# Kernel optimization log

Hardware: AMD Instinct MI355X
Metric: run time of the kernel (lower is better)

## Reference

```python
import jax, jax.numpy as jnp
import numpy as np

D = 256          # descriptor_dim
H = 4            # num heads in AttentionPropagation
DH = D // H
SCALE = 0.1      # hparams['scale_factor']
THR = 0.2        # hparams['match_threshold']
NAMES = ['GATs', 'self', 'cross'] * 4


def conv1d(x, w, b):
    # 1x1 Conv1d == per-position matmul. x:[b,c,n] w:[o,c] b:[o]
    return jnp.einsum('oc,bcn->bon', w, x) + b[None, :, None]


def instnorm(x, eps=1e-5):
    # torch InstanceNorm1d (affine=False): normalize over spatial dim per channel
    mu = jnp.mean(x, axis=2, keepdims=True)
    var = jnp.var(x, axis=2, keepdims=True)
    return (x - mu) * jax.lax.rsqrt(var + eps)


def linear_attention(q, k, v):
    # q:[b,dh,h,nq] k,v:[b,dh,h,ns]
    eps = 1e-6
    q = jax.nn.elu(q) + 1.0
    k = jax.nn.elu(k) + 1.0
    m = v.shape[3]
    v = v / m
    KV = jnp.einsum('bdhm,bqhm->bqdh', k, v)
    Z = 1.0 / (jnp.einsum('bdhm,bdh->bhm', q, k.sum(3)) + eps)
    return jnp.einsum('bdhm,bqdh,bhm->bqhm', q, KV, Z) * m


def mha(x, src, pw, pb, mw, mb):
    b, _, nq = x.shape
    ns = src.shape[2]
    q = conv1d(x, pw[0], pb[0]).reshape(b, DH, H, nq)
    k = conv1d(src, pw[1], pb[1]).reshape(b, DH, H, ns)
    v = conv1d(src, pw[2], pb[2]).reshape(b, DH, H, ns)
    o = linear_attention(q, k, v).reshape(b, D, nq)
    return conv1d(o, mw, mb)


def attn_prop(x, src, pw, pb, mw, mb, w1, b1, w2, b2):
    msg = mha(x, src, pw, pb, mw, mb)
    y = jnp.concatenate([x, msg], axis=1)           # [b, 2D, n]
    y = jax.nn.relu(instnorm(conv1d(y, w1, b1)))
    return conv1d(y, w2, b2)


def gat(d2d, d3d, W, a):
    # GraphAttentionLayer (OnePose): include_self=True, additional=False,
    # with_linear_transform=True, concat=True; dropout inactive at eval.
    # d2d:[b,D,n*L] d3d:[b,D,n]
    b, _, n = d3d.shape
    x2 = jnp.transpose(d2d, (0, 2, 1)).reshape(b, n, -1, D)   # [b,n,L,D]
    x3 = jnp.transpose(d3d, (0, 2, 1))                        # [b,n,D]
    x2 = jnp.concatenate([x3[:, :, None, :], x2], axis=2)     # include self -> L+1
    Wh2 = jnp.einsum('bnld,do->bnlo', x2, W)
    Wh3 = jnp.einsum('bnd,do->bno', x3, W)
    e = jax.nn.leaky_relu(
        jnp.einsum('bno,o->bn', Wh3, a[:D])[:, :, None]
        + jnp.einsum('bnlo,o->bnl', Wh2, a[D:]), 0.2)
    att = jax.nn.softmax(e, axis=-1)
    h = jnp.einsum('bnl,bnld->bnd', att, Wh2)
    return jnp.transpose(jax.nn.elu(h), (0, 2, 1))            # [b,D,n]


def gnn_and_scores(dq, d3, d2db, projw, projb, mergew, mergeb,
                   mlp1w, mlp1b, mlp2w, mlp2b, gatW, gata, finw, finb):
    gi = 0
    ai = 0
    for name in NAMES:
        if name == 'GATs':
            d3 = gat(d2db, d3, gatW[gi], gata[gi])
            gi += 1
        else:
            src0, src1 = (d3, dq) if name == 'cross' else (dq, d3)
            p = (projw[ai], projb[ai], mergew[ai], mergeb[ai],
                 mlp1w[ai], mlp1b[ai], mlp2w[ai], mlp2b[ai])
            dq = dq + attn_prop(dq, src0, *p)
            d3 = d3 + attn_prop(d3, src1, *p)
            ai += 1
    mq = conv1d(dq, finw, finb)
    md = conv1d(d3, finw, finb)
    mq = mq / jnp.maximum(jnp.linalg.norm(mq, axis=1, keepdims=True), 1e-12)
    md = md / jnp.maximum(jnp.linalg.norm(md, axis=1, keepdims=True), 1e-12)
    scores = jnp.einsum('bdn,bdm->bnm', mq, md) / SCALE
    conf = jax.nn.softmax(scores, axis=1) * jax.nn.softmax(scores, axis=2)
    return conf


def setup_inputs() -> dict:
    key = jax.random.key(0)
    ks = jax.random.split(key, 16)
    b, n1, n2, L = 2, 3072, 3072, 8
    s = 0.02
    f32 = jnp.float32
    return {
        'desc2d_query': jax.random.normal(ks[0], (b, D, n1), f32),
        'desc3d_db': jax.random.normal(ks[1], (b, D, n2), f32),
        'desc2d_db': jax.random.normal(ks[2], (b, D, n2 * L), f32),
        'projw': jax.random.normal(ks[3], (8, 3, D, D), f32) * s,
        'projb': jnp.zeros((8, 3, D), f32),
        'mergew': jax.random.normal(ks[4], (8, D, D), f32) * s,
        'mergeb': jnp.zeros((8, D), f32),
        'mlp1w': jax.random.normal(ks[5], (8, 2 * D, 2 * D), f32) * s,
        'mlp1b': jnp.zeros((8, 2 * D), f32),
        'mlp2w': jax.random.normal(ks[6], (8, D, 2 * D), f32) * s,
        'mlp2b': jnp.zeros((8, D), f32),
        'gatW': jax.random.normal(ks[7], (4, D, D), f32) * s,
        'gata': jax.random.normal(ks[8], (4, 2 * D), f32) * s,
        'finw': jax.random.normal(ks[9], (D, D), f32) * s,
        'finb': jnp.zeros((D,), f32),
    }


def reference(desc2d_query, desc3d_db, desc2d_db, projw, projb, mergew, mergeb,
              mlp1w, mlp1b, mlp2w, mlp2b, gatW, gata, finw, finb):
    conf = gnn_and_scores(desc2d_query, desc3d_db, desc2d_db, projw, projb,
                          mergew, mergeb, mlp1w, mlp1b, mlp2w, mlp2b,
                          gatW, gata, finw, finb)
    b, n1, n2 = conf.shape
    i0 = jnp.argmax(conf, axis=2)
    m0 = jnp.max(conf, axis=2)
    i1 = jnp.argmax(conf, axis=1)
    m1 = jnp.max(conf, axis=1)
    mutual0 = jnp.arange(n1)[None] == jnp.take_along_axis(i1, i0, axis=1)
    mutual1 = jnp.arange(n2)[None] == jnp.take_along_axis(i0, i1, axis=1)
    ms0 = jnp.where(mutual0, m0, 0.0)
    ms1 = jnp.where(mutual1, jnp.take_along_axis(ms0, i1, axis=1), 0.0)
    valid0 = mutual0 & (ms0 > THR)
    valid1 = mutual1 & jnp.take_along_axis(valid0, i1, axis=1)
    ind0 = jnp.where(valid0, i0, -1)
    ind1 = jnp.where(valid1, i1, -1)
    return (ind0[0], ind1[0], ms0[0], ms1[0], conf)
```

## Files before the change

### kernel.cpp

```cpp
#include <hip/hip_runtime.h>
#include <hip/hip_bf16.h>
#include <math.h>

typedef long long ll;
typedef __attribute__((ext_vector_type(8))) short s8v;
typedef __attribute__((ext_vector_type(4))) float f4v;
typedef __attribute__((address_space(1))) unsigned int gu32;
typedef __attribute__((address_space(3))) unsigned int lu32;

#define NPOS 3072

#define OFF_STF   0LL
#define OFF_STB   3145728LL
#define OFF_QKV   4718592LL
#define OFF_MSG   9437184LL
#define OFF_HID   11010048LL
#define OFF_WBF   14155776LL
#define OFF_PBP   16941056LL
#define OFF_KV    16947200LL
#define OFF_KSUM  17012736LL
#define OFF_KSP   17013760LL
#define OFF_UVEC  17026048LL
#define OFF_E2ALL 17028096LL
#define OFF_ATT   17224704LL
#define OFF_SVEC  17280000LL
#define OFF_INP   17292288LL
#define OFF_PMAX  17300480LL
#define OFF_PSUM  17595392LL
#define OFF_CMAX  17890304LL
#define OFF_CSUM  17896448LL
#define OFF_CAPV  17902592LL
#define OFF_CAPI  17976320LL
#define OFF_I0    18050048LL
#define OFF_M0    18053120LL
#define OFF_I1    18056192LL
#define OFF_M1B   18059264LL
#define OFF_B1C   18583552LL

__device__ __forceinline__ float b2f(short s) {
  union { unsigned u; float f; } c;
  c.u = ((unsigned)(unsigned short)s) << 16;
  return c.f;
}
__device__ __forceinline__ short f2b(float f) {
  __hip_bfloat16 h = __float2bfloat16(f);
  union { __hip_bfloat16 h; short s; } c; c.h = h; return c.s;
}
__device__ __forceinline__ unsigned pk2(float a, float b) {
  return (unsigned)(unsigned short)f2b(a) | ((unsigned)(unsigned short)f2b(b) << 16);
}
__device__ __forceinline__ float waveSum(float v) {
#pragma unroll
  for (int off = 32; off > 0; off >>= 1) v += __shfl_down(v, off);
  return v;
}
__device__ __forceinline__ void gld16(const short* g, short* l) {
  __builtin_amdgcn_global_load_lds((const gu32*)g, (lu32*)l, 16, 0, 0);
}

__global__ __launch_bounds__(256) void bgemm_k(
    const short* __restrict__ A, const short* __restrict__ A2, int KS,
    int lda, int lda2,
    const short* __restrict__ B,
    const float* __restrict__ bias, const float* __restrict__ R,
    float* __restrict__ C, short* __restrict__ C2,
    const float* __restrict__ rs, const float* __restrict__ cs,
    int K, int ldc, float alpha,
    ll aB, ll a2B, ll bB, ll rB, ll cB, ll c2B,
    int za, int zbo, int act, int zand)
{
  __shared__ __align__(16) short As[2][128 * 32];
  __shared__ __align__(16) short Bs[2][128 * 32];
  const int z = blockIdx.z;
  const int zA = (z + za) & zand, zB = (z + zbo) & zand;
  const int j0 = blockIdx.x * 128, i0 = blockIdx.y * 128;
  const int t = threadIdx.x;
  const int lane = t & 63, w = t >> 6;
  const int wi = (w & 1) * 64, wj = (w >> 1) * 64;
  const int fr = lane & 15;
  const int cl = lane >> 4;
  const int r4 = cl * 4;

  const short* baseA[2]; const short* baseA2[2]; const short* baseB[2];
  int sl[2];
  {
    const short* Az = A + (ll)zA * aB;
    const short* A2z = A2 ? A2 + (ll)zA * a2B : nullptr;
    const short* Bz = B + (ll)zB * bB;
#pragma unroll
    for (int i = 0; i < 2; ++i) {
      int cc = t + i * 256;
      int r = cc >> 2;
      int sq = ((cc & 3) ^ ((r >> 1) & 3)) << 3;
      baseA[i] = Az + (ll)(i0 + r) * lda + sq;
      baseA2[i] = A2 ? A2z + (ll)(i0 + r) * lda2 + sq : nullptr;
      baseB[i] = Bz + (ll)(j0 + r) * K + sq;
      sl[i] = cc << 3;
    }
  }
  int offA[4], offB[4];
#pragma unroll
  for (int im = 0; im < 4; ++im) {
    int ra = wi + im * 16 + fr;
    offA[im] = ra * 32 + ((cl ^ ((ra >> 1) & 3)) << 3);
    int rb = wj + im * 16 + fr;
    offB[im] = rb * 32 + ((cl ^ ((rb >> 1) & 3)) << 3);
  }

  f4v acc[4][4];
#pragma unroll
  for (int i = 0; i < 4; ++i)
#pragma unroll
    for (int j = 0; j < 4; ++j) acc[i][j] = (f4v)0.f;

  const int nt = K >> 5;
#pragma unroll
  for (int i = 0; i < 2; ++i) gld16(baseA[i], As[0] + sl[i]);
#pragma unroll
  for (int i = 0; i < 2; ++i) gld16(baseB[i], Bs[0] + sl[i]);
  __syncthreads();

  for (int kt = 0; kt < nt; ++kt) {
    const int cur = kt & 1;
    if (kt + 1 < nt) {
      const int k0 = (kt + 1) * 32;
      short* dA = As[cur ^ 1]; short* dB = Bs[cur ^ 1];
      if (A2 && k0 >= KS) {
#pragma unroll
        for (int i = 0; i < 2; ++i) gld16(baseA2[i] + (k0 - KS), dA + sl[i]);
      } else {
#pragma unroll
        for (int i = 0; i < 2; ++i) gld16(baseA[i] + k0, dA + sl[i]);
      }
#pragma unroll
      for (int i = 0; i < 2; ++i) gld16(baseB[i] + k0, dB + sl[i]);
    }
    const short* Ac = As[cur]; const short* Bc = Bs[cur];
    s8v af[4], bfr[4];
#pragma unroll
    for (int im = 0; im < 4; ++im) af[im] = *(const s8v*)(Ac + offA[im]);
#pragma unroll
    for (int in = 0; in < 4; ++in) bfr[in] = *(const s8v*)(Bc + offB[in]);
#pragma unroll
    for (int im = 0; im < 4; ++im)
#pragma unroll
      for (int in = 0; in < 4; ++in)
        acc[im][in] = __builtin_amdgcn_mfma_f32_16x16x32_bf16(
            af[im], bfr[in], acc[im][in], 0, 0, 0);
    __syncthreads();
  }

  float* Cz = C ? C + (ll)z * cB : nullptr;
  short* C2z = C2 ? C2 + (ll)z * c2B : nullptr;
  const float* Rz = R ? R + (ll)z * rB : nullptr;
  const float* rsz = rs ? rs + (ll)z * NPOS : nullptr;
  float bv4[4], cv4[4];
#pragma unroll
  for (int in = 0; in < 4; ++in) {
    int j = j0 + wj + in * 16 + fr;
    bv4[in] = bias ? bias[j] : 0.f;
    cv4[in] = cs ? cs[(ll)zB * NPOS + j] : 1.f;
  }
#pragma unroll
  for (int im = 0; im < 4; ++im) {
#pragma unroll
    for (int r = 0; r < 4; ++r) {
      int i = i0 + wi + im * 16 + r4 + r;
      float rsv = rsz ? rsz[i] : 1.f;
      int rowo = i * ldc;
#pragma unroll
      for (int in = 0; in < 4; ++in) {
        int j = j0 + wj + in * 16 + fr;
        float v = acc[im][in][r] * alpha;
        if (rsz) v = v * rsv * cv4[in];
        v += bv4[in];
        int off = rowo + j;
        if (Rz) v += Rz[off];
        if (act) v = v > 0.f ? v : (expf(v) - 1.f);
        if (Cz) Cz[off] = v;
        if (C2z) C2z[off] = f2b(v);
      }
    }
  }
}

__global__ void transpose_in_k(const float* __restrict__ dq, const float* __restrict__ d3,
                               float* __restrict__ stf, short* __restrict__ stb)
{
  __shared__ float tile[64][65];
  int z = blockIdx.z;
  const float* src = (z < 2) ? dq + (ll)z * 786432 : d3 + (ll)(z - 2) * 786432;
  int c0 = blockIdx.y * 64, n0 = blockIdx.x * 64;
  int t = threadIdx.x;
  int nj = t & 63, q = t >> 6;
#pragma unroll
  for (int i = 0; i < 16; ++i) {
    int ci = q + i * 4;
    tile[ci][nj] = src[(ll)(c0 + ci) * NPOS + n0 + nj];
  }
  __syncthreads();
  int cj = t & 63;
#pragma unroll
  for (int i = 0; i < 16; ++i) {
    int ni = q + i * 4;
    float v = tile[cj][ni];
    ll o = (ll)z * 786432 + (ll)(n0 + ni) * 256 + c0 + cj;
    stf[o] = v;
    stb[o] = f2b(v);
  }
}

__global__ void f2b_k(const float* __restrict__ src, short* __restrict__ dst, int n8)
{
  int gi = blockIdx.x * 256 + threadIdx.x;
  if (gi >= n8) return;
  ll e = (ll)gi * 8;
  float4 a = *(const float4*)(src + e);
  float4 b = *(const float4*)(src + e + 4);
  uint4 o;
  o.x = pk2(a.x, a.y); o.y = pk2(a.z, a.w);
  o.z = pk2(b.x, b.y); o.w = pk2(b.z, b.w);
  *(uint4*)(dst + e) = o;
}

__global__ void f2b_split_k(const float* __restrict__ src, short* __restrict__ d1,
                            short* __restrict__ d2)
{
  int gi = blockIdx.x * 256 + threadIdx.x;
  ll e = (ll)gi * 8;
  int k = (int)(e & 511);
  ll row = e >> 9;
  float4 a = *(const float4*)(src + e);
  float4 b = *(const float4*)(src + e + 4);
  uint4 o;
  o.x = pk2(a.x, a.y); o.y = pk2(a.z, a.w);
  o.z = pk2(b.x, b.y); o.w = pk2(b.z, b.w);
  if (k < 256) *(uint4*)(d1 + row * 512 + k) = o;
  else         *(uint4*)(d2 + row * 256 + (k - 256)) = o;
}

__global__ void projw_perm_k(const float* __restrict__ src, short* __restrict__ dst)
{
  int idx = blockIdx.x * 256 + threadIdx.x;
  int c = idx & 255;
  int row = (idx >> 8) % 768;
  int ai = (idx >> 8) / 768;
  int sec = row >> 8;
  int p = row & 255;
  int o = (p & 63) * 4 + (p >> 6);
  dst[idx] = f2b(src[(((ll)ai * 3 + sec) * 256 + o) * 256 + c]);
}

__global__ void pbp_k(const float* __restrict__ pb, float* __restrict__ pbp)
{
  int idx = blockIdx.x * 256 + threadIdx.x;
  int row = idx % 768, ai = idx / 768;
  int sec = row >> 8;
  int p = row & 255;
  int o = (p & 63) * 4 + (p >> 6);
  pbp[idx] = pb[ai * 768 + (sec << 8) + o];
}

__global__ void mergewT_k(const float* __restrict__ src, short* __restrict__ dst)
{
  __shared__ float tile[64][65];
  int ai = blockIdx.z;
  int p0 = blockIdx.x * 64, c0 = blockIdx.y * 64;
  int h = p0 >> 6;
  int t = threadIdx.x;
  int q = t & 63, cq = t >> 6;
#pragma unroll
  for (int i = 0; i < 16; ++i) {
    int cc = cq + i * 4;
    tile[q][cc] = src[(ll)ai * 65536 + (ll)(c0 + cc) * 256 + 4 * q + h];
  }
  __syncthreads();
#pragma unroll
  for (int i = 0; i < 16; ++i) {
    int pi = cq + i * 4;
    dst[((ll)ai * 256 + p0 + pi) * 256 + c0 + q] = f2b(tile[pi][q]);
  }
}

__global__ void biasfold_k(const float* __restrict__ mlp1w, const float* __restrict__ mlp1b,
                           const float* __restrict__ mergeb, float* __restrict__ b1c)
{
  int b = blockIdx.x;
  int ai = b >> 3, o0 = (b & 7) * 64;
  int t = threadIdx.x;
  int w = t >> 6, lane = t & 63;
  float4 mb = *(const float4*)(mergeb + ai * 256 + lane * 4);
#pragma unroll
  for (int ol = 0; ol < 16; ++ol) {
    int o = o0 + w * 16 + ol;
    float4 wv = *(const float4*)(mlp1w + ((ll)(ai * 512 + o)) * 512 + 256 + lane * 4);
    float s = wv.x * mb.x + wv.y * mb.y + wv.z * mb.z + wv.w * mb.w;
    s = waveSum(s);
    if (lane == 0) b1c[ai * 512 + o] = mlp1b[ai * 512 + o] + s;
  }
}

__global__ void gatw_t_k(const float* __restrict__ src, short* __restrict__ dst)
{
  __shared__ float tile[64][65];
  int gi = blockIdx.z;
  int d0 = blockIdx.x * 64, o0 = blockIdx.y * 64;
  int t = threadIdx.x;
  int nj = t & 63, q = t >> 6;
#pragma unroll
  for (int i = 0; i < 16; ++i) {
    int di = q + i * 4;
    tile[di][nj] = src[(ll)gi * 65536 + (ll)(d0 + di) * 256 + o0 + nj];
  }
  __syncthreads();
#pragma unroll
  for (int i = 0; i < 16; ++i) {
    int oi = q + i * 4;
    dst[(ll)gi * 65536 + (ll)(o0 + oi) * 256 + d0 + nj] = f2b(tile[nj][oi]);
  }
}

__global__ void gat_prep_k(const float* __restrict__ gatW, const float* __restrict__ gata,
                           float* __restrict__ uvec)
{
  int gi = blockIdx.x; int d = threadIdx.x;
  const float* W = gatW + (ll)gi * 65536;
  const float* a = gata + gi * 512;
  float u0 = 0.f, u1 = 0.f;
  for (int o = 0; o < 256; o += 4) {
    float4 w4 = *(const float4*)(W + d * 256 + o);
    float4 a4 = *(const float4*)(a + o);
    float4 b4 = *(const float4*)(a + 256 + o);
    u0 += w4.x * a4.x + w4.y * a4.y + w4.z * a4.z + w4.w * a4.w;
    u1 += w4.x * b4.x + w4.y * b4.y + w4.z * b4.z + w4.w * b4.w;
  }
  uvec[gi * 512 + d] = u0;
  uvec[gi * 512 + 256 + d] = u1;
}

__global__ void e2all_k(const float* __restrict__ d2db, const float* __restrict__ uvec,
                        float* __restrict__ e2all)
{
  __shared__ float us[1024];
  int t = threadIdx.x;
  for (int idx = t; idx < 1024; idx += 256)
    us[idx] = uvec[(idx >> 8) * 512 + 256 + (idx & 255)];
  __syncthreads();
  int m = blockIdx.x * 256 + t;
  int b = blockIdx.y;
  const float* xb = d2db + (ll)b * 6291456;
  float a[4] = {};
  for (int c = 0; c < 256; ++c) {
    float v = xb[(ll)c * 24576 + m];
#pragma unroll
    for (int g = 0; g < 4; ++g) a[g] = fmaf(v, us[g * 256 + c], a[g]);
  }
#pragma unroll
  for (int g = 0; g < 4; ++g) e2all[((ll)g * 2 + b) * 24576 + m] = a[g];
}

__global__ void gat_att_k(const short* __restrict__ stb, const float* __restrict__ uvec,
                          const float* __restrict__ e2all, float* __restrict__ att, int gi)
{
  __shared__ float ush[512];
  int t = threadIdx.x;
  for (int idx = t; idx < 512; idx += 256) ush[idx] = uvec[gi * 512 + idx];
  __syncthreads();
  int q = t & 3, pl = t >> 2;
  int n = blockIdx.x * 64 + pl;
  int b = blockIdx.y;
  const short* xr = stb + (ll)(2 + b) * 786432 + (ll)n * 256 + q * 64;
  float a0 = 0.f, a1 = 0.f;
#pragma unroll
  for (int i = 0; i < 8; ++i) {
    s8v v8 = *(const s8v*)(xr + i * 8);
#pragma unroll
    for (int j = 0; j < 8; ++j) {
      float v = b2f(v8[j]);
      a0 = fmaf(v, ush[q * 64 + i * 8 + j], a0);
      a1 = fmaf(v, ush[256 + q * 64 + i * 8 + j], a1);
    }
  }
  a0 += __shfl_xor(a0, 1); a0 += __shfl_xor(a0, 2);
  a1 += __shfl_xor(a1, 1); a1 += __shfl_xor(a1, 2);
  if (q == 0) {
    float e[9];
    e[0] = a0 + a1;
    const float* e2b = e2all + ((ll)gi * 2 + b) * 24576 + (ll)n * 8;
#pragma unroll
    for (int l = 0; l < 8; ++l) e[l + 1] = a0 + e2b[l];
    float mx = -3.4e38f;
#pragma unroll
    for (int l = 0; l < 9; ++l) {
      e[l] = e[l] >= 0.f ? e[l] : 0.2f * e[l];
      mx = fmaxf(mx, e[l]);
    }
    float s = 0.f;
#pragma unroll
    for (int l = 0; l < 9; ++l) { e[l] = expf(e[l] - mx); s += e[l]; }
    float inv = 1.f / s;
    float* ao = att + ((ll)b * NPOS + n) * 9;
#pragma unroll
    for (int l = 0; l < 9; ++l) ao[l] = e[l] * inv;
  }
}

__global__ __launch_bounds__(256) void gat_g_k(
    const short* __restrict__ stb, const float* __restrict__ d2db,
    const float* __restrict__ att, short* __restrict__ g)
{
  __shared__ float attw[576];
  __shared__ float gtile[64 * 69];
  const int n0 = blockIdx.x * 64, c0 = blockIdx.y * 64, b = blockIdx.z;
  const int t = threadIdx.x;
  for (int idx = t; idx < 576; idx += 256)
    attw[idx] = att[((ll)b * NPOS + n0) * 9 + idx];
  __syncthreads();
  const int nl = t >> 2, l2 = (t & 3) * 2;
  for (int cc = 0; cc < 64; ++cc) {
    const float* src = d2db + ((ll)b * 256 + c0 + cc) * 24576 + (ll)n0 * 8;
    float2 v = *(const float2*)(src + t * 2);
    float p = v.x * attw[nl * 9 + 1 + l2] + v.y * attw[nl * 9 + 2 + l2];
    p += __shfl_xor(p, 1);
    p += __shfl_xor(p, 2);
    if ((t & 3) == 0) gtile[nl * 69 + cc] = p;
  }
  __syncthreads();
#pragma unroll
  for (int i = 0; i < 4; ++i) {
    int n = (t >> 4) + i * 16;
    int cp = (t & 15) * 4;
    float at0 = attw[n * 9];
    const short* dr = stb + (ll)(2 + b) * 786432 + (ll)(n0 + n) * 256 + c0 + cp;
    uint2 dv = *(const uint2*)dr;
    float d0 = b2f((short)(dv.x & 0xffff)), d1 = b2f((short)(dv.x >> 16));
    float d2 = b2f((short)(dv.y & 0xffff)), d3v = b2f((short)(dv.y >> 16));
    uint2 ov;
    ov.x = pk2(gtile[n * 69 + cp] + at0 * d0, gtile[n * 69 + cp + 1] + at0 * d1);
    ov.y = pk2(gtile[n * 69 + cp + 2] + at0 * d2, gtile[n * 69 + cp + 3] + at0 * d3v);
    *(uint2*)(g + (ll)b * 786432 + (ll)(n0 + n) * 256 + c0 + cp) = ov;
  }
}

__global__ __launch_bounds__(256) void kv_partial_k(
    const short* __restrict__ qkv, float* __restrict__ kvp, float* __restrict__ ksp)
{
  __shared__ float ks[32][66];
  __shared__ float vs[32][66];
  const int p = blockIdx.x, h = blockIdx.y, z = blockIdx.z;
  const short* base = qkv + (ll)z * 2359296;
  const int t = threadIdx.x;
  const int tq = (t >> 4) * 4, tk = (t & 15) * 4;
  const int ml = t >> 3, d8 = (t & 7) * 8;
  float acc[4][4] = {};
  float ksl = 0.f;
  for (int sub = 0; sub < 8; ++sub) {
    int m0 = p * 256 + sub * 32;
    {
      const short* kr = base + (ll)(m0 + ml) * 768 + 256 + h * 64 + d8;
      s8v k8 = *(const s8v*)kr;
      s8v v8 = *(const s8v*)(kr + 256);
#pragma unroll
      for (int j = 0; j < 8; ++j) {
        float kvv = b2f(k8[j]);
        ks[ml][d8 + j] = kvv > 0.f ? kvv + 1.f : expf(kvv);
        vs[ml][d8 + j] = b2f(v8[j]);
      }
    }
    __syncthreads();
#pragma unroll 8
    for (int mm = 0; mm < 32; ++mm) {
      float vv[4], kk[4];
#pragma unroll
      for (int i = 0; i < 4; ++i) { vv[i] = vs[mm][tq + i]; kk[i] = ks[mm][tk + i]; }
#pragma unroll
      for (int i = 0; i < 4; ++i)
#pragma unroll
        for (int j = 0; j < 4; ++j)
          acc[i][j] = fmaf(vv[i], kk[j], acc[i][j]);
    }
    if (t < 64) {
#pragma unroll 8
      for (int mm = 0; mm < 32; ++mm) ksl += ks[mm][t];
    }
    __syncthreads();
  }
  ll o = (((ll)z * 4 + h) * 12 + p) * 4096;
#pragma unroll
  for (int i = 0; i < 4; ++i)
    *(float4*)(kvp + o + (tq + i) * 64 + tk) =
        make_float4(acc[i][0], acc[i][1], acc[i][2], acc[i][3]);
  if (t < 64) ksp[(((ll)z * 4 + h) * 12 + p) * 64 + t] = ksl;
}

__global__ void kv_reduce_k(const float* __restrict__ kvp, const float* __restrict__ ksp,
                            float* __restrict__ kv, float* __restrict__ ksum)
{
  int bh = blockIdx.x; int t = threadIdx.x;
  int e0 = blockIdx.y * 1024;
  for (int e = e0 + t; e < e0 + 1024; e += 256) {
    float s = 0.f;
    for (int p = 0; p < 12; ++p) s += kvp[((ll)bh * 12 + p) * 4096 + e];
    kv[(ll)bh * 4096 + (ll)(e & 63) * 64 + (e >> 6)] = s;
  }
  if (blockIdx.y == 0 && t < 64) {
    float s = 0.f;
    for (int p = 0; p < 12; ++p) s += ksp[((ll)bh * 12 + p) * 64 + t];
    ksum[bh * 64 + t] = s;
  }
}

__global__ __launch_bounds__(256) void attn_out_k(
    const short* __restrict__ qkv, const float* __restrict__ kv,
    const float* __restrict__ ksum, short* __restrict__ obuf)
{
  __shared__ float qt[64][67];
  __shared__ float kvT[64][66];
  __shared__ float zsh[64];
  __shared__ float kss[64];
  const int n0 = blockIdx.x * 64, h = blockIdx.y, z = blockIdx.z;
  const int t = threadIdx.x;
  {
    int nl = t >> 3, d8 = (t & 7) * 8;
    const short* qr0 = qkv + (ll)z * 2359296 + (ll)(n0 + nl) * 768 + h * 64 + d8;
#pragma unroll
    for (int i = 0; i < 2; ++i) {
      const short* qr = qr0 + (ll)i * 32 * 768;
      s8v q8 = *(const s8v*)qr;
#pragma unroll
      for (int j = 0; j < 8; ++j) {
        float q = b2f(q8[j]);
        qt[nl + i * 32][d8 + j] = q > 0.f ? q + 1.f : expf(q);
      }
    }
  }
  {
    const float* kvb = kv + (ll)(z * 4 + h) * 4096;
#pragma unroll
    for (int i = 0; i < 16; ++i) {
      int idx = t + i * 256;
      kvT[idx >> 6][idx & 63] = kvb[idx];
    }
  }
  if (t < 64) kss[t] = ksum[(z * 4 + h) * 64 + t];
  __syncthreads();
  if (t < 64) {
    float s = 0.f;
    for (int d = 0; d < 64; ++d) s = fmaf(qt[t][d], kss[d], s);
    zsh[t] = 1.f / (s + 1e-6f);
  }
  __syncthreads();
  const int tn = t >> 4, tj = t & 15;
  float acc[4][4] = {};
  for (int d = 0; d < 64; ++d) {
    float av[4], bv[4];
#pragma unroll
    for (int i = 0; i < 4; ++i) av[i] = qt[tn * 4 + i][d];
    *(float4*)bv = *(const float4*)&kvT[d][tj * 4];
#pragma unroll
    for (int i = 0; i < 4; ++i)
#pragma unroll
      for (int j = 0; j < 4; ++j)
        acc[i][j] = fmaf(av[i], bv[j], acc[i][j]);
  }
#pragma unroll
  for (int i = 0; i < 4; ++i) {
    int n = n0 + tn * 4 + i;
    float zv = zsh[tn * 4 + i];
    uint2 o;
    o.x = pk2(acc[i][0] * zv, acc[i][1] * zv);
    o.y = pk2(acc[i][2] * zv, acc[i][3] * zv);
    *(uint2*)(obuf + (ll)z * 786432 + (ll)n * 256 + h * 64 + tj * 4) = o;
  }
}

__global__ void in_part_k(const short* __restrict__ hid, float* __restrict__ part)
{
  int z = blockIdx.z, cg = blockIdx.y, nc = blockIdx.x;
  int t = threadIdx.x;
  int c = cg * 64 + (t & 63);
  const short* base = hid + (ll)z * 1572864 + (ll)(nc * 384 + (t >> 6)) * 512 + c;
  float s = 0.f, q = 0.f;
#pragma unroll 4
  for (int i = 0; i < 96; ++i) {
    float v = b2f(base[(ll)i * 2048]);
    s += v; q = fmaf(v, v, q);
  }
  __shared__ float rs_[4][64], rq_[4][64];
  rs_[t >> 6][t & 63] = s; rq_[t >> 6][t & 63] = q;
  __syncthreads();
  if (t < 64) {
    s = rs_[0][t] + rs_[1][t] + rs_[2][t] + rs_[3][t];
    q = rq_[0][t] + rq_[1][t] + rq_[2][t] + rq_[3][t];
    ll o = ((((ll)z * 8 + cg) * 8 + nc) * 64 + t) * 2;
    part[o] = s; part[o + 1] = q;
  }
}

__global__ void in_apply_k(short* __restrict__ hid, const float* __restrict__ part)
{
  int z = blockIdx.z, cg = blockIdx.y, nc = blockIdx.x;
  int t = threadIdx.x;
  int c = cg * 64 + (t & 63);
  float s = 0.f, q = 0.f;
#pragma unroll
  for (int p = 0; p < 8; ++p) {
    ll o = ((((ll)z * 8 + cg) * 8 + p) * 64 + (t & 63)) * 2;
    s += part[o]; q += part[o + 1];
  }
  float mu = s * (1.f / NPOS);
  float var = q * (1.f / NPOS) - mu * mu;
  float rsig = rsqrtf(fmaxf(var, 0.f) + 1e-5f);
  short* base = hid + (ll)z * 1572864 + (ll)(nc * 384 + (t >> 6)) * 512 + c;
#pragma unroll 4
  for (int i = 0; i < 96; ++i) {
    float v = (b2f(base[(ll)i * 2048]) - mu) * rsig;
    base[(ll)i * 2048] = f2b(v > 0.f ? v : 0.f);
  }
}

__global__ void normcalc_k(const short* __restrict__ f, float* __restrict__ svec)
{
  int n = blockIdx.x * 256 + threadIdx.x;
  int z = blockIdx.y;
  const short* r = f + (ll)z * 786432 + (ll)n * 256;
  float s = 0.f;
#pragma unroll 8
  for (int i = 0; i < 32; ++i) {
    s8v v8 = *(const s8v*)(r + i * 8);
#pragma unroll
    for (int j = 0; j < 8; ++j) { float v = b2f(v8[j]); s = fmaf(v, v, s); }
  }
  svec[z * NPOS + n] = 1.f / fmaxf(sqrtf(s), 1e-12f);
}

__global__ void colstat_part_k(const float* __restrict__ S,
                               float* __restrict__ pmax, float* __restrict__ psum)
{
  int m = blockIdx.x * 256 + threadIdx.x;
  int chunk = blockIdx.y; int b = blockIdx.z;
  const float* base = S + (ll)b * 9437184 + m;
  float mx = -3.4e38f, s = 0.f;
  int n0 = chunk * 64;
  for (int n = n0; n < n0 + 64; ++n) {
    float v = base[(ll)n * NPOS];
    if (v > mx) { s = s * expf(mx - v) + 1.f; mx = v; }
    else s += expf(v - mx);
  }
  ll o = ((ll)b * 48 + chunk) * NPOS + m;
  pmax[o] = mx; psum[o] = s;
}

__global__ void colstat_comb_k(const float* __restrict__ pmax, const float* __restrict__ psum,
                               float* __restrict__ cmax, float* __restrict__ csum)
{
  int m = blockIdx.x * 256 + threadIdx.x; int b = blockIdx.y;
  float M = -3.4e38f;
  for (int c = 0; c < 48; ++c) M = fmaxf(M, pmax[((ll)b * 48 + c) * NPOS + m]);
  float s = 0.f;
  for (int c = 0; c < 48; ++c)
    s += psum[((ll)b * 48 + c) * NPOS + m] * expf(pmax[((ll)b * 48 + c) * NPOS + m] - M);
  cmax[b * NPOS + m] = M; csum[b * NPOS + m] = s;
}

__global__ __launch_bounds__(256) void rowfix_k(
    float* __restrict__ S, const float* __restrict__ cmax, const float* __restrict__ csum,
    int* __restrict__ i0, float* __restrict__ m0)
{
  int n = blockIdx.x, b = blockIdx.y, t = threadIdx.x;
  float* row = S + (ll)b * 9437184 + (ll)n * NPOS;
  __shared__ float red[4];
  float v[12];
  float mx = -3.4e38f;
#pragma unroll
  for (int i = 0; i < 12; ++i) { v[i] = row[t + i * 256]; mx = fmaxf(mx, v[i]); }
#pragma unroll
  for (int off = 32; off > 0; off >>= 1) mx = fmaxf(mx, __shfl_down(mx, off));
  if ((t & 63) == 0) red[t >> 6] = mx;
  __syncthreads();
  float rm = fmaxf(fmaxf(red[0], red[1]), fmaxf(red[2], red[3]));
  __syncthreads();
  float s = 0.f;
#pragma unroll
  for (int i = 0; i < 12; ++i) s += expf(v[i] - rm);
  s = waveSum(s);
  if ((t & 63) == 0) red[t >> 6] = s;
  __syncthreads();
  float irs = 1.f / (red[0] + red[1] + red[2] + red[3]);
  float bv = -1.f; int bi = 0;
#pragma unroll
  for (int i = 0; i < 12; ++i) {
    int m = t + i * 256;
    float f = expf(2.f * v[i] - rm - cmax[b * NPOS + m]) * irs / csum[b * NPOS + m];
    row[m] = f;
    if (f > bv) { bv = f; bi = m; }
  }
  if (b == 0) {
#pragma unroll
    for (int off = 32; off > 0; off >>= 1) {
      float ov = __shfl_down(bv, off);
      int oi = __shfl_down(bi, off);
      if (ov > bv || (ov == bv && oi < bi)) { bv = ov; bi = oi; }
    }
    __shared__ float rv[4]; __shared__ int ri[4];
    if ((t & 63) == 0) { rv[t >> 6] = bv; ri[t >> 6] = bi; }
    __syncthreads();
    if (t == 0) {
      for (int w = 1; w < 4; ++w)
        if (rv[w] > bv || (rv[w] == bv && ri[w] < bi)) { bv = rv[w]; bi = ri[w]; }
      i0[n] = bi; m0[n] = bv;
    }
  }
}

__global__ void colamax_part_k(const float* __restrict__ Cf,
                               float* __restrict__ capv, int* __restrict__ capi)
{
  int m = blockIdx.x * 256 + threadIdx.x;
  int n0 = blockIdx.y * 128;
  float bv = -1.f; int bi = 0;
  for (int n = n0; n < n0 + 128; ++n) {
    float f = Cf[(ll)n * NPOS + m];
    if (f > bv) { bv = f; bi = n; }
  }
  capv[blockIdx.y * NPOS + m] = bv;
  capi[blockIdx.y * NPOS + m] = bi;
}

__global__ void colamax_comb_k(const float* __restrict__ capv, const int* __restrict__ capi,
                               int* __restrict__ i1)
{
  int m = blockIdx.x * 256 + threadIdx.x;
  float bv = -1.f; int bi = 0;
  for (int c = 0; c < 24; ++c) {
    float v = capv[c * NPOS + m];
    if (v > bv) { bv = v; bi = capi[c * NPOS + m]; }
  }
  i1[m] = bi;
}

__global__ void match0_k(const int* __restrict__ i0, const float* __restrict__ m0,
                         const int* __restrict__ i1, float* __restrict__ out)
{
  int n = blockIdx.x * 256 + threadIdx.x;
  int j = i0[n];
  bool mut = (i1[j] == n);
  float ms0 = mut ? m0[n] : 0.f;
  bool valid = mut && (ms0 > 0.2f);
  out[n] = valid ? (float)j : -1.f;
  out[6144 + n] = ms0;
}

__global__ void match1_k(const int* __restrict__ i0, const int* __restrict__ i1,
                         float* __restrict__ out)
{
  int m = blockIdx.x * 256 + threadIdx.x;
  int j = i1[m];
  bool mut = (i0[j] == m);
  float ms0v = out[6144 + j];
  float ind0v = out[j];
  float ms1 = mut ? ms0v : 0.f;
  bool valid1 = mut && (ind0v >= 0.f);
  out[3072 + m] = valid1 ? (float)j : -1.f;
  out[9216 + m] = ms1;
}

extern "C" void kernel_launch(void* const* d_in, const int* in_sizes, int n_in,
                              void* d_out, int out_size, void* d_ws, size_t ws_size,
                              hipStream_t stream)
{
  const float* desc2dq = (const float*)d_in[0];
  const float* desc3db = (const float*)d_in[1];
  const float* desc2db = (const float*)d_in[2];
  const float* projw = (const float*)d_in[3];
  const float* projb = (const float*)d_in[4];
  const float* mergew = (const float*)d_in[5];
  const float* mergeb = (const float*)d_in[6];
  const float* mlp1w = (const float*)d_in[7];
  const float* mlp1b = (const float*)d_in[8];
  const float* mlp2w = (const float*)d_in[9];
  const float* mlp2b = (const float*)d_in[10];
  const float* gatW = (const float*)d_in[11];
  const float* gata = (const float*)d_in[12];
  const float* finw = (const float*)d_in[13];
  const float* finb = (const float*)d_in[14];

  float* ws = (float*)d_ws;
  float* out = (float*)d_out;

  float* stf = ws + OFF_STF;
  short* stb = (short*)(ws + OFF_STB);
  short* qkv = (short*)(ws + OFF_QKV);
  short* msg = (short*)(ws + OFF_MSG);
  short* obuf = msg;
  short* hid = (short*)(ws + OFF_HID);
  float* kvp = ws + OFF_HID + 1572864;
  short* wbf = (short*)(ws + OFF_WBF);
  short* projw_bf = wbf;
  short* mergewT_bf = wbf + 1572864;
  short* mlp1c_bf = wbf + 2097152;
  short* mlp2w_bf = wbf + 4194304;
  short* gatwT_bf = wbf + 5242880;
  short* finw_bf = wbf + 5505024;
  float* pbp = ws + OFF_PBP;
  float* kvb = ws + OFF_KV;
  float* ksum = ws + OFF_KSUM;
  float* ksp = ws + OFF_KSP;
  float* uvec = ws + OFF_UVEC;
  float* e2all = ws + OFF_E2ALL;
  float* att = ws + OFF_ATT;
  float* svec = ws + OFF_SVEC;
  float* inp = ws + OFF_INP;
  float* pmax = ws + OFF_PMAX;
  float* psum = ws + OFF_PSUM;
  float* cmax = ws + OFF_CMAX;
  float* csum = ws + OFF_CSUM;
  float* capv = ws + OFF_CAPV;
  int* capi = (int*)(ws + OFF_CAPI);
  int* i0 = (int*)(ws + OFF_I0);
  float* m0 = ws + OFF_M0;
  int* i1 = (int*)(ws + OFF_I1);
  short* m1b_bf = (short*)(ws + OFF_M1B);
  float* b1c = ws + OFF_B1C;
  short* finbf = msg;

  auto bgemm = [&](const short* A, const short* A2, int KS, int lda, int lda2,
                   const short* B, const float* bias, const float* R,
                   float* C, short* C2, const float* rsc, const float* csc,
                   int J, int K, int ldc, float alpha,
                   ll aB, ll a2B, ll bB, ll rB, ll cB, ll c2B,
                   int za, int zbo, int act, int nz) {
    bgemm_k<<<dim3(J / 128, 24, nz), 256, 0, stream>>>(
        A, A2, KS, lda, lda2, B, bias, R, C, C2, rsc, csc,
        K, ldc, alpha, aB, a2B, bB, rB, cB, c2B, za, zbo, act, 3);
  };

  transpose_in_k<<<dim3(48, 4, 4), 256, 0, stream>>>(desc2dq, desc3db, stf, stb);
  projw_perm_k<<<6144, 256, 0, stream>>>(projw, projw_bf);
  pbp_k<<<24, 256, 0, stream>>>(projb, pbp);
  mergewT_k<<<dim3(4, 4, 8), 256, 0, stream>>>(mergew, mergewT_bf);
  f2b_split_k<<<1024, 256, 0, stream>>>(mlp1w, mlp1c_bf, m1b_bf);
  f2b_k<<<512, 256, 0, stream>>>(mlp2w, mlp2w_bf, 131072);
  gatw_t_k<<<dim3(4, 4, 4), 256, 0, stream>>>(gatW, gatwT_bf);
  f2b_k<<<32, 256, 0, stream>>>(finw, finw_bf, 8192);
  biasfold_k<<<64, 256, 0, stream>>>(mlp1w, mlp1b, mergeb, b1c);
  bgemm_k<<<dim3(2, 4, 8), 256, 0, stream>>>(
      m1b_bf, nullptr, 0, 256, 0, mergewT_bf, nullptr, nullptr,
      nullptr, mlp1c_bf + 256, nullptr, nullptr,
      256, 512, 1.f, 131072, 0, 65536, 0, 0, 262144, 0, 0, 0, 7);
  gat_prep_k<<<4, 256, 0, stream>>>(gatW, gata, uvec);
  e2all_k<<<dim3(96, 2), 256, 0, stream>>>(desc2db, uvec, e2all);

  auto attn_layer = [&](int ai, int cross) {
    const short* pw = projw_bf + (ll)ai * 196608;
    const float* pb = pbp + (ll)ai * 768;
    if (!cross) {
      bgemm(stb, nullptr, 0, 256, 0, pw, pb, nullptr, nullptr, qkv, nullptr, nullptr,
            768, 256, 768, 1.f, 786432, 0, 0, 0, 0, 2359296, 0, 0, 0, 4);
    } else {
      bgemm(stb, nullptr, 0, 256, 0, pw, pb, nullptr, nullptr, qkv, nullptr, nullptr,
            256, 256, 768, 1.f, 786432, 0, 0, 0, 0, 2359296, 0, 0, 0, 4);
      bgemm(stb, nullptr, 0, 256, 0, pw + 65536, pb + 256, nullptr, nullptr, qkv + 256,
            nullptr, nullptr,
            512, 256, 768, 1.f, 786432, 0, 0, 0, 0, 2359296, 2, 0, 0, 4);
    }
    kv_partial_k<<<dim3(12, 4, 4), 256, 0, stream>>>(qkv, kvp, ksp);
    kv_reduce_k<<<dim3(16, 4), 256, 0, stream>>>(kvp, ksp, kvb, ksum);
    attn_out_k<<<dim3(48, 4, 4), 256, 0, stream>>>(qkv, kvb, ksum, obuf);
    bgemm(stb, obuf, 256, 256, 256, mlp1c_bf + (ll)ai * 262144, b1c + (ll)ai * 512,
          nullptr, nullptr, hid, nullptr, nullptr,
          512, 512, 512, 1.f, 786432, 786432, 0, 0, 0, 1572864, 0, 0, 0, 4);
    in_part_k<<<dim3(8, 8, 4), 256, 0, stream>>>(hid, inp);
    in_apply_k<<<dim3(8, 8, 4), 256, 0, stream>>>(hid, inp);
    bgemm(hid, nullptr, 0, 512, 0, mlp2w_bf + (ll)ai * 131072, mlp2b + (ll)ai * 256,
          stf, stf, stb, nullptr, nullptr,
          256, 512, 256, 1.f, 1572864, 0, 0, 786432, 786432, 786432, 0, 0, 0, 4);
  };

  auto gat_layer = [&](int gi) {
    gat_att_k<<<dim3(48, 2), 256, 0, stream>>>(stb, uvec, e2all, att, gi);
    gat_g_k<<<dim3(48, 4, 2), 256, 0, stream>>>(stb, desc2db, att, obuf);
    bgemm(obuf, nullptr, 0, 256, 0, gatwT_bf + (ll)gi * 65536, nullptr, nullptr,
          stf + (ll)2 * 786432, stb + (ll)2 * 786432, nullptr, nullptr,
          256, 256, 256, 1.f, 786432, 0, 0, 0, 786432, 786432, 0, 0, 1, 2);
  };

  int ai = 0, gi = 0;
  for (int r = 0; r < 4; ++r) {
    gat_layer(gi); gi++;
    attn_layer(ai, 0); ai++;
    attn_layer(ai, 1); ai++;
  }

  bgemm(stb, nullptr, 0, 256, 0, finw_bf, finb, nullptr, nullptr, finbf, nullptr, nullptr,
        256, 256, 256, 1.f, 786432, 0, 0, 0, 0, 786432, 0, 0, 0, 4);
  normcalc_k<<<dim3(12, 4), 256, 0, stream>>>(finbf, svec);

  float* conf = out + 12288;
  bgemm(finbf, nullptr, 0, 256, 0, finbf, nullptr, nullptr, conf, nullptr, svec, svec,
        3072, 256, 3072, 10.f, 786432, 0, 786432, 0, 9437184, 0, 0, 2, 0, 2);

  colstat_part_k<<<dim3(12, 48, 2), 256, 0, stream>>>(conf, pmax, psum);
  colstat_comb_k<<<dim3(12, 2), 256, 0, stream>>>(pmax, psum, cmax, csum);
  rowfix_k<<<dim3(NPOS, 2), 256, 0, stream>>>(conf, cmax, csum, i0, m0);
  colamax_part_k<<<dim3(12, 24), 256, 0, stream>>>(conf, capv, capi);
  colamax_comb_k<<<12, 256, 0, stream>>>(capv, capi, i1);
  match0_k<<<12, 256, 0, stream>>>(i0, m0, i1, out);
  match1_k<<<12, 256, 0, stream>>>(i0, i1, out);
}
```

Measured before the change: 1.750 ms.

## Template GEMM tiles and add three-stage LDS pipeline with explicit waitcnt

Turns the bf16 MFMA GEMM into a template over tile rows, tile columns and K depth. Every call site now uses smaller 64x128 or 64x64 tiles, which gives more blocks per launch on a grid of 3072 rows. The LDS double buffer becomes a triple buffer with two tiles prefetched, explicit vmcnt waits and raw barriers, so global loads overlap more with MFMA work, and the K loop is fully unrolled. The smaller tiles cost some operand reuse, and the hand-written waitcnt and barrier ordering must be exactly right to avoid races.

```diff
diff --git a/kernel.cpp b/kernel.cpp
--- a/kernel.cpp
+++ b/kernel.cpp
@@ -57,7 +57,14 @@
 __device__ __forceinline__ void gld16(const short* g, short* l) {
   __builtin_amdgcn_global_load_lds((const gu32*)g, (lu32*)l, 16, 0, 0);
 }
-
+template<int N> __device__ __forceinline__ void wvm() {
+  asm volatile("s_waitcnt vmcnt(%0)" :: "n"(N) : "memory");
+}
+__device__ __forceinline__ void wlgk0() {
+  asm volatile("s_waitcnt lgkmcnt(0)" ::: "memory");
+}
+
+template<int BI, int BJ, int KT>
 __global__ __launch_bounds__(256) void bgemm_k(
     const short* __restrict__ A, const short* __restrict__ A2, int KS,
     int lda, int lda2,
@@ -65,111 +72,133 @@
     const float* __restrict__ bias, const float* __restrict__ R,
     float* __restrict__ C, short* __restrict__ C2,
     const float* __restrict__ rs, const float* __restrict__ cs,
-    int K, int ldc, float alpha,
+    int ldc, float alpha,
     ll aB, ll a2B, ll bB, ll rB, ll cB, ll c2B,
     int za, int zbo, int act, int zand)
 {
-  __shared__ __align__(16) short As[2][128 * 32];
-  __shared__ __align__(16) short Bs[2][128 * 32];
+  constexpr int NT = KT / 32;
+  constexpr int WI = (BI == 128) ? 2 : 1;
+  constexpr int JW = BJ / (4 / WI);
+  constexpr int FI = (BI / WI) / 16;
+  constexpr int FJ = JW / 16;
+  constexpr int SA = BI / 64, SB = BJ / 64;
+  constexpr int LPT = SA + SB;
+  __shared__ __align__(16) short As[3][BI * 32];
+  __shared__ __align__(16) short Bs[3][BJ * 32];
   const int z = blockIdx.z;
   const int zA = (z + za) & zand, zB = (z + zbo) & zand;
-  const int j0 = blockIdx.x * 128, i0 = blockIdx.y * 128;
+  const int j0 = blockIdx.x * BJ, i0 = blockIdx.y * BI;
   const int t = threadIdx.x;
   const int lane = t & 63, w = t >> 6;
-  const int wi = (w & 1) * 64, wj = (w >> 1) * 64;
+  const int wi = (WI == 2) ? (w & 1) * 64 : 0;
+  const int wj = (WI == 2) ? (w >> 1) * JW : w * JW;
   const int fr = lane & 15;
   const int cl = lane >> 4;
   const int r4 = cl * 4;
 
-  const short* baseA[2]; const short* baseA2[2]; const short* baseB[2];
-  int sl[2];
+  const short* baseA[SA]; const short* baseA2[SA]; const short* baseB[SB];
+  int slA[SA], slB[SB];
   {
     const short* Az = A + (ll)zA * aB;
     const short* A2z = A2 ? A2 + (ll)zA * a2B : nullptr;
     const short* Bz = B + (ll)zB * bB;
 #pragma unroll
-    for (int i = 0; i < 2; ++i) {
+    for (int i = 0; i < SA; ++i) {
       int cc = t + i * 256;
       int r = cc >> 2;
       int sq = ((cc & 3) ^ ((r >> 1) & 3)) << 3;
       baseA[i] = Az + (ll)(i0 + r) * lda + sq;
       baseA2[i] = A2 ? A2z + (ll)(i0 + r) * lda2 + sq : nullptr;
-      baseB[i] = Bz + (ll)(j0 + r) * K + sq;
-      sl[i] = cc << 3;
-    }
-  }
-  int offA[4], offB[4];
-#pragma unroll
-  for (int im = 0; im < 4; ++im) {
+      slA[i] = cc << 3;
+    }
+#pragma unroll
+    for (int i = 0; i < SB; ++i) {
+      int cc = t + i * 256;
+      int r = cc >> 2;
+      int sq = ((cc & 3) ^ ((r >> 1) & 3)) << 3;
+      baseB[i] = Bz + (ll)(j0 + r) * KT + sq;
+      slB[i] = cc << 3;
+    }
+  }
+  int offA[FI], offB[FJ];
+#pragma unroll
+  for (int im = 0; im < FI; ++im) {
     int ra = wi + im * 16 + fr;
     offA[im] = ra * 32 + ((cl ^ ((ra >> 1) & 3)) << 3);
-    int rb = wj + im * 16 + fr;
-    offB[im] = rb * 32 + ((cl ^ ((rb >> 1) & 3)) << 3);
-  }
-
-  f4v acc[4][4];
-#pragma unroll
-  for (int i = 0; i < 4; ++i)
-#pragma unroll
-    for (int j = 0; j < 4; ++j) acc[i][j] = (f4v)0.f;
-
-  const int nt = K >> 5;
-#pragma unroll
-  for (int i = 0; i < 2; ++i) gld16(baseA[i], As[0] + sl[i]);
-#pragma unroll
-  for (int i = 0; i < 2; ++i) gld16(baseB[i], Bs[0] + sl[i]);
-  __syncthreads();
-
-  for (int kt = 0; kt < nt; ++kt) {
-    const int cur = kt & 1;
-    if (kt + 1 < nt) {
-      const int k0 = (kt + 1) * 32;
-      short* dA = As[cur ^ 1]; short* dB = Bs[cur ^ 1];
-      if (A2 && k0 >= KS) {
-#pragma unroll
-        for (int i = 0; i < 2; ++i) gld16(baseA2[i] + (k0 - KS), dA + sl[i]);
-      } else {
-#pragma unroll
-        for (int i = 0; i < 2; ++i) gld16(baseA[i] + k0, dA + sl[i]);
-      }
-#pragma unroll
-      for (int i = 0; i < 2; ++i) gld16(baseB[i] + k0, dB + sl[i]);
-    }
-    const short* Ac = As[cur]; const short* Bc = Bs[cur];
-    s8v af[4], bfr[4];
-#pragma unroll
-    for (int im = 0; im < 4; ++im) af[im] = *(const s8v*)(Ac + offA[im]);
-#pragma unroll
-    for (int in = 0; in < 4; ++in) bfr[in] = *(const s8v*)(Bc + offB[in]);
-#pragma unroll
-    for (int im = 0; im < 4; ++im)
-#pragma unroll
-      for (int in = 0; in < 4; ++in)
+  }
+#pragma unroll
+  for (int in = 0; in < FJ; ++in) {
+    int rb = wj + in * 16 + fr;
+    offB[in] = rb * 32 + ((cl ^ ((rb >> 1) & 3)) << 3);
+  }
+
+  f4v acc[FI][FJ];
+#pragma unroll
+  for (int i = 0; i < FI; ++i)
+#pragma unroll
+    for (int j = 0; j < FJ; ++j) acc[i][j] = (f4v)0.f;
+
+  auto stage = [&](int tile, int bi_) {
+    const int k0 = tile * 32;
+    short* dA = As[bi_]; short* dB = Bs[bi_];
+    if (A2 && k0 >= KS) {
+#pragma unroll
+      for (int i = 0; i < SA; ++i) gld16(baseA2[i] + (k0 - KS), dA + slA[i]);
+    } else {
+#pragma unroll
+      for (int i = 0; i < SA; ++i) gld16(baseA[i] + k0, dA + slA[i]);
+    }
+#pragma unroll
+    for (int i = 0; i < SB; ++i) gld16(baseB[i] + k0, dB + slB[i]);
+  };
+
+  stage(0, 0);
+  stage(1, 1);
+#pragma unroll
+  for (int kt = 0; kt < NT; ++kt) {
+    if (kt + 2 < NT) { stage(kt + 2, (kt + 2) % 3); wvm<2 * LPT>(); }
+    else if (kt + 1 < NT) { wvm<LPT>(); }
+    else { wvm<0>(); }
+    __builtin_amdgcn_s_barrier();
+    asm volatile("" ::: "memory");
+    const short* Ac = As[kt % 3]; const short* Bc = Bs[kt % 3];
+    s8v af[FI], bfr[FJ];
+#pragma unroll
+    for (int im = 0; im < FI; ++im) af[im] = *(const s8v*)(Ac + offA[im]);
+#pragma unroll
+    for (int in = 0; in < FJ; ++in) bfr[in] = *(const s8v*)(Bc + offB[in]);
+#pragma unroll
+    for (int im = 0; im < FI; ++im)
+#pragma unroll
+      for (int in = 0; in < FJ; ++in)
         acc[im][in] = __builtin_amdgcn_mfma_f32_16x16x32_bf16(
             af[im], bfr[in], acc[im][in], 0, 0, 0);
-    __syncthreads();
+    if (kt + 1 < NT) {
+      wlgk0();
+      __builtin_amdgcn_s_barrier();
+    }
   }
 
   float* Cz = C ? C + (ll)z * cB : nullptr;
   short* C2z = C2 ? C2 + (ll)z * c2B : nullptr;
   const float* Rz = R ? R + (ll)z * rB : nullptr;
   const float* rsz = rs ? rs + (ll)z * NPOS : nullptr;
-  float bv4[4], cv4[4];
-#pragma unroll
-  for (int in = 0; in < 4; ++in) {
+  float bv4[FJ], cv4[FJ];
+#pragma unroll
+  for (int in = 0; in < FJ; ++in) {
     int j = j0 + wj + in * 16 + fr;
     bv4[in] = bias ? bias[j] : 0.f;
     cv4[in] = cs ? cs[(ll)zB * NPOS + j] : 1.f;
   }
 #pragma unroll
-  for (int im = 0; im < 4; ++im) {
+  for (int im = 0; im < FI; ++im) {
 #pragma unroll
     for (int r = 0; r < 4; ++r) {
       int i = i0 + wi + im * 16 + r4 + r;
       float rsv = rsz ? rsz[i] : 1.f;
       int rowo = i * ldc;
 #pragma unroll
-      for (int in = 0; in < 4; ++in) {
+      for (int in = 0; in < FJ; ++in) {
         int j = j0 + wj + in * 16 + fr;
         float v = acc[im][in][r] * alpha;
         if (rsz) v = v * rsv * cv4[in];
@@ -824,17 +853,6 @@
   float* b1c = ws + OFF_B1C;
   short* finbf = msg;
 
-  auto bgemm = [&](const short* A, const short* A2, int KS, int lda, int lda2,
-                   const short* B, const float* bias, const float* R,
-                   float* C, short* C2, const float* rsc, const float* csc,
-                   int J, int K, int ldc, float alpha,
-                   ll aB, ll a2B, ll bB, ll rB, ll cB, ll c2B,
-                   int za, int zbo, int act, int nz) {
-    bgemm_k<<<dim3(J / 128, 24, nz), 256, 0, stream>>>(
-        A, A2, KS, lda, lda2, B, bias, R, C, C2, rsc, csc,
-        K, ldc, alpha, aB, a2B, bB, rB, cB, c2B, za, zbo, act, 3);
-  };
-
   transpose_in_k<<<dim3(48, 4, 4), 256, 0, stream>>>(desc2dq, desc3db, stf, stb);
   projw_perm_k<<<6144, 256, 0, stream>>>(projw, projw_bf);
   pbp_k<<<24, 256, 0, stream>>>(projb, pbp);
@@ -844,10 +862,10 @@
   gatw_t_k<<<dim3(4, 4, 4), 256, 0, stream>>>(gatW, gatwT_bf);
   f2b_k<<<32, 256, 0, stream>>>(finw, finw_bf, 8192);
   biasfold_k<<<64, 256, 0, stream>>>(mlp1w, mlp1b, mergeb, b1c);
-  bgemm_k<<<dim3(2, 4, 8), 256, 0, stream>>>(
+  bgemm_k<64, 128, 256><<<dim3(2, 8, 8), 256, 0, stream>>>(
       m1b_bf, nullptr, 0, 256, 0, mergewT_bf, nullptr, nullptr,
       nullptr, mlp1c_bf + 256, nullptr, nullptr,
-      256, 512, 1.f, 131072, 0, 65536, 0, 0, 262144, 0, 0, 0, 7);
+      512, 1.f, 131072, 0, 65536, 0, 0, 262144, 0, 0, 0, 7);
   gat_prep_k<<<4, 256, 0, stream>>>(gatW, gata, uvec);
   e2all_k<<<dim3(96, 2), 256, 0, stream>>>(desc2db, uvec, e2all);
 
@@ -855,34 +873,40 @@
     const short* pw = projw_bf + (ll)ai * 196608;
     const float* pb = pbp + (ll)ai * 768;
     if (!cross) {
-      bgemm(stb, nullptr, 0, 256, 0, pw, pb, nullptr, nullptr, qkv, nullptr, nullptr,
-            768, 256, 768, 1.f, 786432, 0, 0, 0, 0, 2359296, 0, 0, 0, 4);
+      bgemm_k<64, 128, 256><<<dim3(6, 48, 4), 256, 0, stream>>>(
+          stb, nullptr, 0, 256, 0, pw, pb, nullptr, nullptr, qkv, nullptr, nullptr,
+          768, 1.f, 786432, 0, 0, 0, 0, 2359296, 0, 0, 0, 3);
     } else {
-      bgemm(stb, nullptr, 0, 256, 0, pw, pb, nullptr, nullptr, qkv, nullptr, nullptr,
-            256, 256, 768, 1.f, 786432, 0, 0, 0, 0, 2359296, 0, 0, 0, 4);
-      bgemm(stb, nullptr, 0, 256, 0, pw + 65536, pb + 256, nullptr, nullptr, qkv + 256,
-            nullptr, nullptr,
-            512, 256, 768, 1.f, 786432, 0, 0, 0, 0, 2359296, 2, 0, 0, 4);
+      bgemm_k<64, 64, 256><<<dim3(4, 48, 4), 256, 0, stream>>>(
+          stb, nullptr, 0, 256, 0, pw, pb, nullptr, nullptr, qkv, nullptr, nullptr,
+          768, 1.f, 786432, 0, 0, 0, 0, 2359296, 0, 0, 0, 3);
+      bgemm_k<64, 128, 256><<<dim3(4, 48, 4), 256, 0, stream>>>(
+          stb, nullptr, 0, 256, 0, pw + 65536, pb + 256, nullptr, nullptr, qkv + 256,
+          nullptr, nullptr,
+          768, 1.f, 786432, 0, 0, 0, 0, 2359296, 2, 0, 0, 3);
     }
     kv_partial_k<<<dim3(12, 4, 4), 256, 0, stream>>>(qkv, kvp, ksp);
     kv_reduce_k<<<dim3(16, 4), 256, 0, stream>>>(kvp, ksp, kvb, ksum);
     attn_out_k<<<dim3(48, 4, 4), 256, 0, stream>>>(qkv, kvb, ksum, obuf);
-    bgemm(stb, obuf, 256, 256, 256, mlp1c_bf + (ll)ai * 262144, b1c + (ll)ai * 512,
-          nullptr, nullptr, hid, nullptr, nullptr,
-          512, 512, 512, 1.f, 786432, 786432, 0, 0, 0, 1572864, 0, 0, 0, 4);
+    bgemm_k<64, 128, 512><<<dim3(4, 48, 4), 256, 0, stream>>>(
+        stb, obuf, 256, 256, 256, mlp1c_bf + (ll)ai * 262144, b1c + (ll)ai * 512,
+        nullptr, nullptr, hid, nullptr, nullptr,
+        512, 1.f, 786432, 786432, 0, 0, 0, 1572864, 0, 0, 0, 3);
     in_part_k<<<dim3(8, 8, 4), 256, 0, stream>>>(hid, inp);
     in_apply_k<<<dim3(8, 8, 4), 256, 0, stream>>>(hid, inp);
-    bgemm(hid, nullptr, 0, 512, 0, mlp2w_bf + (ll)ai * 131072, mlp2b + (ll)ai * 256,
-          stf, stf, stb, nullptr, nullptr,
-          256, 512, 256, 1.f, 1572864, 0, 0, 786432, 786432, 786432, 0, 0, 0, 4);
+    bgemm_k<64, 64, 512><<<dim3(4, 48, 4), 256, 0, stream>>>(
+        hid, nullptr, 0, 512, 0, mlp2w_bf + (ll)ai * 131072, mlp2b + (ll)ai * 256,
+        stf, stf, stb, nullptr, nullptr,
+        256, 1.f, 1572864, 0, 0, 786432, 786432, 786432, 0, 0, 0, 3);
   };
 
   auto gat_layer = [&](int gi) {
     gat_att_k<<<dim3(48, 2), 256, 0, stream>>>(stb, uvec, e2all, att, gi);
     gat_g_k<<<dim3(48, 4, 2), 256, 0, stream>>>(stb, desc2db, att, obuf);
-    bgemm(obuf, nullptr, 0, 256, 0, gatwT_bf + (ll)gi * 65536, nullptr, nullptr,
-          stf + (ll)2 * 786432, stb + (ll)2 * 786432, nullptr, nullptr,
-          256, 256, 256, 1.f, 786432, 0, 0, 0, 786432, 786432, 0, 0, 1, 2);
+    bgemm_k<64, 64, 256><<<dim3(4, 48, 2), 256, 0, stream>>>(
+        obuf, nullptr, 0, 256, 0, gatwT_bf + (ll)gi * 65536, nullptr, nullptr,
+        stf + (ll)2 * 786432, stb + (ll)2 * 786432, nullptr, nullptr,
+        256, 1.f, 786432, 0, 0, 0, 786432, 786432, 0, 0, 1, 3);
   };
 
   int ai = 0, gi = 0;
@@ -892,13 +916,15 @@
     attn_layer(ai, 1); ai++;
   }
 
-  bgemm(stb, nullptr, 0, 256, 0, finw_bf, finb, nullptr, nullptr, finbf, nullptr, nullptr,
-        256, 256, 256, 1.f, 786432, 0, 0, 0, 0, 786432, 0, 0, 0, 4);
+  bgemm_k<64, 64, 256><<<dim3(4, 48, 4), 256, 0, stream>>>(
+      stb, nullptr, 0, 256, 0, finw_bf, finb, nullptr, nullptr, finbf, nullptr, nullptr,
+      256, 1.f, 786432, 0, 0, 0, 0, 786432, 0, 0, 0, 3);
   normcalc_k<<<dim3(12, 4), 256, 0, stream>>>(finbf, svec);
 
   float* conf = out + 12288;
-  bgemm(finbf, nullptr, 0, 256, 0, finbf, nullptr, nullptr, conf, nullptr, svec, svec,
-        3072, 256, 3072, 10.f, 786432, 0, 786432, 0, 9437184, 0, 0, 2, 0, 2);
+  bgemm_k<64, 128, 256><<<dim3(24, 48, 2), 256, 0, stream>>>(
+      finbf, nullptr, 0, 256, 0, finbf, nullptr, nullptr, conf, nullptr, svec, svec,
+      3072, 10.f, 786432, 0, 786432, 0, 9437184, 0, 0, 2, 0, 3);
 
   colstat_part_k<<<dim3(12, 48, 2), 256, 0, stream>>>(conf, pmax, psum);
   colstat_comb_k<<<dim3(12, 2), 256, 0, stream>>>(pmax, psum, cmax, csum);
```

New measurement: 1.526 ms. -12.8%, faster.
